# Optimization experiments

Hardware: AMD Instinct MI355X
Metric: run time of the kernel (lower is better)

The kernel has to match this reference:

```python
import jax, jax.numpy as jnp
import numpy as np

N_NODES = 32768
N_GRAPHS = 8
NODES_PER_GRAPH = N_NODES // N_GRAPHS
DEG = 8
N_EDGES = N_NODES * DEG
TW = 25
H = 128
N_LAYERS = 6
L_PDE = 16.0
TMAX = 4.0
DT = 0.04
EPS = 1e-5


def swish(x):
    return x * jax.nn.sigmoid(x)


def _lin(k, fin, fout):
    kw, kb = jax.random.split(k)
    s = 1.0 / np.sqrt(fin)
    return (jax.random.uniform(kw, (fin, fout), minval=-s, maxval=s),
            jax.random.uniform(kb, (fout,), minval=-s, maxval=s))


def _lin_stack(k, n, fin, fout):
    Ws, bs = [], []
    for kk in jax.random.split(k, n):
        W, b = _lin(kk, fin, fout)
        Ws.append(W); bs.append(b)
    return jnp.stack(Ws), jnp.stack(bs)


def setup_inputs() -> dict:
    key = jax.random.key(0)
    ks = jax.random.split(key, 16)
    emb_in = 2 * TW + 2        # 52 = u(50) + pos_x(1) + pos_t(1)
    msg_in = 2 * H + 2 * TW + 2  # 308 = x_i,x_j,u_i-u_j,dpos_x,vars_i
    upd_in = 2 * H + 1          # 257 = x, message, vars
    inp = {}
    inp['u'] = jax.random.normal(ks[0], (N_NODES, 2 * TW), dtype=jnp.float32)
    pos_t = jax.random.uniform(ks[1], (N_NODES, 1)) * TMAX
    pos_x = jax.random.uniform(ks[2], (N_NODES, 1)) * L_PDE
    inp['pos'] = jnp.concatenate([pos_t, pos_x], axis=-1)
    src = jax.random.randint(ks[3], (N_EDGES,), 0, N_NODES)
    dst = jnp.repeat(jnp.arange(N_NODES), DEG)  # every node gets DEG in-edges
    inp['edge_index'] = jnp.stack([src, dst]).astype(jnp.int32)
    inp['batch_idx'] = (jnp.arange(N_NODES) // NODES_PER_GRAPH).astype(jnp.int32)
    inp['emb_W1'], inp['emb_b1'] = _lin(ks[4], emb_in, H)
    inp['emb_W2'], inp['emb_b2'] = _lin(ks[5], H, H)
    inp['msg1_W'], inp['msg1_b'] = _lin_stack(ks[6], N_LAYERS, msg_in, H)
    inp['msg2_W'], inp['msg2_b'] = _lin_stack(ks[7], N_LAYERS, H, H)
    inp['upd1_W'], inp['upd1_b'] = _lin_stack(ks[8], N_LAYERS, upd_in, H)
    inp['upd2_W'], inp['upd2_b'] = _lin_stack(ks[9], N_LAYERS, H, H)
    inp['dbl_W'], inp['dbl_b'] = _lin(ks[10], H, 2 * H)
    kc = jax.random.split(ks[11], 4)
    s1 = 1.0 / np.sqrt(2 * 16)
    inp['conv1_W'] = jax.random.uniform(kc[0], (8, 2, 16), minval=-s1, maxval=s1)
    inp['conv1_b'] = jax.random.uniform(kc[1], (8,), minval=-s1, maxval=s1)
    s2 = 1.0 / np.sqrt(8 * 14)
    inp['conv2_W'] = jax.random.uniform(kc[2], (2, 8, 14), minval=-s2, maxval=s2)
    inp['conv2_b'] = jax.random.uniform(kc[3], (2,), minval=-s2, maxval=s2)
    return inp


def reference(u, pos, edge_index, batch_idx, emb_W1, emb_b1, emb_W2, emb_b2,
              msg1_W, msg1_b, msg2_W, msg2_b, upd1_W, upd1_b, upd2_W, upd2_b,
              dbl_W, dbl_b, conv1_W, conv1_b, conv2_W, conv2_b):
    src, dst = edge_index[0], edge_index[1]  # PyG: x_j = x[src], x_i = x[dst]
    pos_x = pos[:, 1:2] / L_PDE
    pos_t = pos[:, 0:1] / TMAX
    variables = pos_t  # eq_variables == {} -> only pos_t
    node_in = jnp.concatenate([u, pos_x, variables], axis=-1)  # [N,52]
    h = swish(swish(node_in @ emb_W1 + emb_b1) @ emb_W2 + emb_b2)
    ones_e = jnp.ones((src.shape[0], 1), u.dtype)
    counts = jnp.maximum(jax.ops.segment_sum(ones_e, dst, N_NODES), 1.0)
    ones_n = jnp.ones((N_NODES, 1), u.dtype)
    gcounts = jax.ops.segment_sum(ones_n, batch_idx, N_GRAPHS)
    u_d = u[dst] - u[src]
    px_d = pos_x[dst] - pos_x[src]
    var_i = variables[dst]

    def layer(hc, p):
        Wm1, bm1, Wm2, bm2, Wu1, bu1, Wu2, bu2 = p
        edge_in = jnp.concatenate([hc[dst], hc[src], u_d, px_d, var_i], -1)  # [E,308]
        m = swish(edge_in @ Wm1 + bm1)
        m = swish(m @ Wm2 + bm2)
        agg = jax.ops.segment_sum(m, dst, N_NODES) / counts  # mean aggregation
        up = swish(jnp.concatenate([hc, agg, variables], -1) @ Wu1 + bu1)
        up = swish(up @ Wu2 + bu2)
        hn = hc + up  # residual (in_features == out_features)
        gm = jax.ops.segment_sum(hn, batch_idx, N_GRAPHS) / gcounts
        hd = hn - gm[batch_idx]
        gv = jax.ops.segment_sum(hd * hd, batch_idx, N_GRAPHS) / gcounts
        return hd * jax.lax.rsqrt(gv + EPS)[batch_idx], None

    h, _ = jax.lax.scan(layer, h, (msg1_W, msg1_b, msg2_W, msg2_b,
                                   upd1_W, upd1_b, upd2_W, upd2_b))
    x2 = swish(h @ dbl_W + dbl_b).reshape(N_NODES, 2, H)  # double_mlp + Unflatten
    dn = ('NCH', 'OIH', 'NCH')
    y = jax.lax.conv_general_dilated(x2, conv1_W, (3,), 'VALID', dimension_numbers=dn)
    y = swish(y + conv1_b[None, :, None])  # [N,8,38]
    diff = jax.lax.conv_general_dilated(y, conv2_W, (1,), 'VALID', dimension_numbers=dn)
    diff = diff + conv2_b[None, :, None]  # [N,2,25]
    dt_cum = DT * jnp.arange(1, TW + 1, dtype=u.dtype)  # cumsum(dt*ones)
    out = u.reshape(N_NODES, 2, TW) + dt_cum[None, None, :] * diff
    return out.reshape(N_NODES, 2 * TW)
```

## Files before the change

kernel.cpp:

```cpp
#include <hip/hip_runtime.h>
#include <hip/hip_bf16.h>

#define N_NODES 32768
#define N_GRAPHS 8
#define NPG 4096
#define DEG 8
#define N_EDGES (N_NODES*DEG)
#define TW 25
#define NL 6
#define L_PDE 16.0f
#define TMAXC 4.0f
#define DTC 0.04f
#define EPSC 1e-5f

typedef __bf16 bf16x8 __attribute__((ext_vector_type(8)));
typedef float f32x4 __attribute__((ext_vector_type(4)));
typedef unsigned short u16;
typedef unsigned int u32;

__device__ __forceinline__ float bf2f(u16 h){
  union { float f; u32 u; } v; v.u = ((u32)h) << 16; return v.f;
}
__device__ __forceinline__ u16 f2bf(float f){
  union { float f; u32 u; } v; v.f = f;
  u32 r = v.u + 0x7FFFu + ((v.u >> 16) & 1u);
  return (u16)(r >> 16);
}
__device__ __forceinline__ float swishf(float x){
  return x / (1.0f + __expf(-x));
}

__global__ void prep_std(const float* __restrict__ src, u16* __restrict__ dst,
                         int Ksrc, int KPAD, int NOUT)
{
  int l = blockIdx.y;
  int per = KPAD * NOUT;
  int i = blockIdx.x * 256 + threadIdx.x;
  if (i >= per) return;
  int KSTEPS = KPAD / 32;
  int e = i & 7;
  int lane = (i >> 3) & 63;
  int ks = (i >> 9) % KSTEPS;
  int nf = i / (KSTEPS * 512);
  int c = nf * 16 + (lane & 15);
  int k = ks * 32 + (lane >> 4) * 8 + e;
  float v = (k < Ksrc) ? src[(size_t)l * Ksrc * NOUT + (size_t)k * NOUT + c] : 0.f;
  dst[(size_t)l * per + i] = f2bf(v);
}

__global__ void prep_AB(const float* __restrict__ W, const float* __restrict__ bsrc,
                        u16* __restrict__ dst, float* __restrict__ bdst)
{
  int l = blockIdx.y;
  const int KSTEPS = 6;
  int i = blockIdx.x * 256 + threadIdx.x;
  int e = i & 7, lane = (i >> 3) & 63, ks = (i >> 9) % KSTEPS, nf = i / (KSTEPS * 512);
  int c = nf * 16 + (lane & 15);
  int k = ks * 32 + (lane >> 4) * 8 + e;
  const float* Wl = W + (size_t)l * 308 * 128;
  float v = 0.f;
  if (c < 128) {
    int rowi = -1;
    if (k < 128) rowi = k;
    else if (k < 178) rowi = 256 + (k - 128);
    else if (k == 178) rowi = 306;
    else if (k == 179) rowi = 307;
    if (rowi >= 0) v = Wl[rowi * 128 + c];
  } else {
    int cc = c - 128; float sgn = 1.f; int rowi = -1;
    if (k < 128) rowi = 128 + k;
    else if (k < 178) { rowi = 256 + (k - 128); sgn = -1.f; }
    else if (k == 178) { rowi = 306; sgn = -1.f; }
    if (rowi >= 0) v = sgn * Wl[rowi * 128 + cc];
  }
  dst[(size_t)l * 192 * 256 + i] = f2bf(v);
  if (i < 256) bdst[l * 256 + i] = (i < 128) ? bsrc[l * 128 + i] : 0.f;
}

__global__ __launch_bounds__(256) void build_static(
    const float* __restrict__ u, const float* __restrict__ pos,
    u16* __restrict__ X0)
{
  int idx = blockIdx.x * 256 + threadIdx.x;
  int n = idx >> 6, j = idx & 63;
  float v;
  if (j < 50) v = u[n * 50 + j];
  else if (j == 50) v = pos[n * 2 + 1] * (1.f / L_PDE);
  else if (j == 51) v = pos[n * 2 + 0] * (1.f / TMAXC);
  else v = 0.f;
  X0[n * 64 + j] = f2bf(v);
}

template<int KPAD, int NOUT, int ACT, int SMODE, int RESID, int HASOUT>
__global__ __launch_bounds__(256) void gemm2(
    const u16* __restrict__ X, int ldx,
    const u16* __restrict__ Xaux,
    float* hB,
    const float* __restrict__ S1p, const float* __restrict__ S2p,
    const float* __restrict__ pos,
    const u16* __restrict__ Wf, const float* __restrict__ bias,
    u16* __restrict__ out, int ldo,
    float* __restrict__ outF,
    float* __restrict__ S1n, float* __restrict__ S2n)
{
  constexpr int KSTEPS = KPAD / 32;
  constexpr int NF2 = NOUT / 32;
  constexpr int CHUNKS = KPAD / 8;
  constexpr int LDO_S = NOUT + 8;
  constexpr int SMEM_US = 64 * (HASOUT ? (KPAD > LDO_S ? KPAD : LDO_S) : KPAD);
  __shared__ u16 sm[SMEM_US];
  int tid = threadIdx.x, lane = tid & 63, wid = tid >> 6;
  int n0 = blockIdx.x * 64;
  int g = n0 >> 12;

  for (int c = tid; c < 64 * CHUNKS; c += 256) {
    int r = c / CHUNKS, kc = c % CHUNKS;
    int n = n0 + r;
    union { uint4 v; u16 s[8]; } o;
    if (SMODE == 0) {
      o.v = *(const uint4*)(X + (size_t)n * ldx + kc * 8);
    } else {
      if (kc < 16) {
        const float* hp = hB + (size_t)n * 128 + kc * 8;
        float4 a0 = *(const float4*)hp, a1 = *(const float4*)(hp + 4);
        float xv[8] = {a0.x,a0.y,a0.z,a0.w,a1.x,a1.y,a1.z,a1.w};
        if (S1p) {
          #pragma unroll
          for (int j = 0; j < 8; ++j) {
            int cc = kc * 8 + j;
            float m = S1p[g * 128 + cc] * (1.f / NPG);
            float var = S2p[g * 128 + cc] * (1.f / NPG) - m * m;
            xv[j] = (xv[j] - m) * rsqrtf(var + EPSC);
          }
        }
        #pragma unroll
        for (int j = 0; j < 8; ++j) o.s[j] = f2bf(xv[j]);
      } else {
        o.v = *(const uint4*)(Xaux + (size_t)n * 64 + (kc - 16) * 8);
      }
    }
    int byte = r * (KPAD * 2) + kc * 16; byte ^= ((r & 7) << 4);
    *(uint4*)((char*)sm + byte) = o.v;
  }
  __syncthreads();

  int rowHalf = wid & 1, colHalf = wid >> 1;
  f32x4 acc[2][NF2];
  f32x4 zero = {0.f, 0.f, 0.f, 0.f};
  #pragma unroll
  for (int m = 0; m < 2; ++m)
    #pragma unroll
    for (int i = 0; i < NF2; ++i) acc[m][i] = zero;
  int rowA = rowHalf * 32 + (lane & 15);
  int kb = lane >> 4;
  #pragma unroll
  for (int ks = 0; ks < KSTEPS; ++ks) {
    int ab0 = rowA * (KPAD * 2) + ks * 64 + kb * 16; ab0 ^= ((rowA & 7) << 4);
    int rA1 = rowA + 16;
    int ab1 = rA1 * (KPAD * 2) + ks * 64 + kb * 16; ab1 ^= ((rA1 & 7) << 4);
    bf16x8 a0 = *(const bf16x8*)((const char*)sm + ab0);
    bf16x8 a1 = *(const bf16x8*)((const char*)sm + ab1);
    #pragma unroll
    for (int nf2 = 0; nf2 < NF2; ++nf2) {
      bf16x8 b = *(const bf16x8*)(Wf + (((colHalf * NF2 + nf2) * KSTEPS + ks) * 64 + lane) * 8);
      acc[0][nf2] = __builtin_amdgcn_mfma_f32_16x16x32_bf16(a0, b, acc[0][nf2], 0, 0, 0);
      acc[1][nf2] = __builtin_amdgcn_mfma_f32_16x16x32_bf16(a1, b, acc[1][nf2], 0, 0, 0);
    }
  }

  if (HASOUT) __syncthreads();
  #pragma unroll
  for (int nf2 = 0; nf2 < NF2; ++nf2) {
    int col = colHalf * (NOUT / 2) + nf2 * 16 + (lane & 15);
    float bv = bias[col];
    #pragma unroll
    for (int m = 0; m < 2; ++m)
      #pragma unroll
      for (int j = 0; j < 4; ++j) {
        int r = rowHalf * 32 + m * 16 + (lane >> 4) * 4 + j;
        float v = acc[m][nf2][j] + bv;
        if (ACT == 1) v = swishf(v);
        if (HASOUT) sm[r * LDO_S + col] = f2bf(v);
        if (outF) outF[(size_t)(n0 + r) * NOUT + col] = v;
      }
  }
  if (HASOUT) {
    __syncthreads();
    for (int c = tid; c < 64 * NOUT / 8; c += 256) {
      int r = c / (NOUT / 8), kc = c % (NOUT / 8);
      uint4 v = *(const uint4*)(sm + r * LDO_S + kc * 8);
      *(uint4*)(out + (size_t)(n0 + r) * ldo + kc * 8) = v;
    }
  }
}

__global__ __launch_bounds__(256) void enc_fused(
    const u16* __restrict__ X0,
    const u16* __restrict__ W1f, const float* __restrict__ b1,
    const u16* __restrict__ W2f, const float* __restrict__ b2,
    float* __restrict__ hB)
{
  __shared__ u16 s1[64 * 64];
  __shared__ u16 s2[64 * 128];
  int tid = threadIdx.x, lane = tid & 63, wid = tid >> 6;
  int n0 = blockIdx.x * 64;

  for (int c = tid; c < 64 * 8; c += 256) {
    int r = c >> 3, kc = c & 7;
    uint4 v = *(const uint4*)(X0 + (size_t)(n0 + r) * 64 + kc * 8);
    int byte = r * 128 + kc * 16; byte ^= ((r & 7) << 4);
    *(uint4*)((char*)s1 + byte) = v;
  }
  __syncthreads();

  int rowHalf = wid & 1, colHalf = wid >> 1;
  int rowA = rowHalf * 32 + (lane & 15), kb = lane >> 4;
  f32x4 acc[2][4];
  f32x4 zero = {0.f, 0.f, 0.f, 0.f};
  #pragma unroll
  for (int m = 0; m < 2; ++m)
    #pragma unroll
    for (int i = 0; i < 4; ++i) acc[m][i] = zero;
  #pragma unroll
  for (int ks = 0; ks < 2; ++ks) {
    int ab0 = rowA * 128 + ks * 64 + kb * 16; ab0 ^= ((rowA & 7) << 4);
    int rA1 = rowA + 16;
    int ab1 = rA1 * 128 + ks * 64 + kb * 16; ab1 ^= ((rA1 & 7) << 4);
    bf16x8 a0 = *(const bf16x8*)((const char*)s1 + ab0);
    bf16x8 a1 = *(const bf16x8*)((const char*)s1 + ab1);
    #pragma unroll
    for (int nf2 = 0; nf2 < 4; ++nf2) {
      bf16x8 b = *(const bf16x8*)(W1f + (((colHalf * 4 + nf2) * 2 + ks) * 64 + lane) * 8);
      acc[0][nf2] = __builtin_amdgcn_mfma_f32_16x16x32_bf16(a0, b, acc[0][nf2], 0, 0, 0);
      acc[1][nf2] = __builtin_amdgcn_mfma_f32_16x16x32_bf16(a1, b, acc[1][nf2], 0, 0, 0);
    }
  }
  #pragma unroll
  for (int nf2 = 0; nf2 < 4; ++nf2) {
    int col = colHalf * 64 + nf2 * 16 + (lane & 15);
    float bv = b1[col];
    #pragma unroll
    for (int m = 0; m < 2; ++m)
      #pragma unroll
      for (int j = 0; j < 4; ++j) {
        int r = rowHalf * 32 + m * 16 + (lane >> 4) * 4 + j;
        int byte = r * 256 + col * 2; byte ^= ((r & 7) << 4);
        *(u16*)((char*)s2 + byte) = f2bf(swishf(acc[m][nf2][j] + bv));
      }
  }
  __syncthreads();
  #pragma unroll
  for (int m = 0; m < 2; ++m)
    #pragma unroll
    for (int i = 0; i < 4; ++i) acc[m][i] = zero;
  #pragma unroll
  for (int ks = 0; ks < 4; ++ks) {
    int ab0 = rowA * 256 + ks * 64 + kb * 16; ab0 ^= ((rowA & 7) << 4);
    int rA1 = rowA + 16;
    int ab1 = rA1 * 256 + ks * 64 + kb * 16; ab1 ^= ((rA1 & 7) << 4);
    bf16x8 a0 = *(const bf16x8*)((const char*)s2 + ab0);
    bf16x8 a1 = *(const bf16x8*)((const char*)s2 + ab1);
    #pragma unroll
    for (int nf2 = 0; nf2 < 4; ++nf2) {
      bf16x8 b = *(const bf16x8*)(W2f + (((colHalf * 4 + nf2) * 4 + ks) * 64 + lane) * 8);
      acc[0][nf2] = __builtin_amdgcn_mfma_f32_16x16x32_bf16(a0, b, acc[0][nf2], 0, 0, 0);
      acc[1][nf2] = __builtin_amdgcn_mfma_f32_16x16x32_bf16(a1, b, acc[1][nf2], 0, 0, 0);
    }
  }
  #pragma unroll
  for (int nf2 = 0; nf2 < 4; ++nf2) {
    int col = colHalf * 64 + nf2 * 16 + (lane & 15);
    float bv = b2[col];
    #pragma unroll
    for (int m = 0; m < 2; ++m)
      #pragma unroll
      for (int j = 0; j < 4; ++j) {
        int r = rowHalf * 32 + m * 16 + (lane >> 4) * 4 + j;
        hB[(size_t)(n0 + r) * 128 + col] = swishf(acc[m][nf2][j] + bv);
      }
  }
}

__global__ __launch_bounds__(256) void upd_fused(
    const u16* __restrict__ Agg,
    float* hB,
    const float* __restrict__ S1p, const float* __restrict__ S2p,
    const float* __restrict__ pos,
    const u16* __restrict__ W1f, const float* __restrict__ b1,
    const u16* __restrict__ W2f, const float* __restrict__ b2,
    float* __restrict__ S1n, float* __restrict__ S2n)
{
  __shared__ u16 s1[64 * 320];
  __shared__ u16 s2[64 * 128];
  int tid = threadIdx.x, lane = tid & 63, wid = tid >> 6;
  int n0 = blockIdx.x * 64;
  int g = n0 >> 12;

  for (int c = tid; c < 64 * 40; c += 256) {
    int r = c / 40, kc = c % 40;
    int n = n0 + r;
    union { uint4 v; u16 s[8]; } o;
    if (kc < 16) {
      const float* hp = hB + (size_t)n * 128 + kc * 8;
      float4 a0 = *(const float4*)hp, a1 = *(const float4*)(hp + 4);
      float xv[8] = {a0.x,a0.y,a0.z,a0.w,a1.x,a1.y,a1.z,a1.w};
      if (S1p) {
        #pragma unroll
        for (int j = 0; j < 8; ++j) {
          int cc = kc * 8 + j;
          float m = S1p[g * 128 + cc] * (1.f / NPG);
          float var = S2p[g * 128 + cc] * (1.f / NPG) - m * m;
          xv[j] = (xv[j] - m) * rsqrtf(var + EPSC);
        }
      }
      #pragma unroll
      for (int j = 0; j < 8; ++j) o.s[j] = f2bf(xv[j]);
    } else if (kc < 32) {
      o.v = *(const uint4*)(Agg + (size_t)n * 128 + (kc - 16) * 8);
    } else {
      #pragma unroll
      for (int j = 0; j < 8; ++j) o.s[j] = 0;
      if (kc == 32) o.s[0] = f2bf(pos[n * 2] * (1.f / TMAXC));
    }
    int byte = r * 640 + kc * 16; byte ^= ((r & 7) << 4);
    *(uint4*)((char*)s1 + byte) = o.v;
  }
  __syncthreads();

  int rowHalf = wid & 1, colHalf = wid >> 1;
  int rowA = rowHalf * 32 + (lane & 15), kb = lane >> 4;
  f32x4 acc[2][4];
  f32x4 zero = {0.f, 0.f, 0.f, 0.f};
  #pragma unroll
  for (int m = 0; m < 2; ++m)
    #pragma unroll
    for (int i = 0; i < 4; ++i) acc[m][i] = zero;
  #pragma unroll
  for (int ks = 0; ks < 10; ++ks) {
    int ab0 = rowA * 640 + ks * 64 + kb * 16; ab0 ^= ((rowA & 7) << 4);
    int rA1 = rowA + 16;
    int ab1 = rA1 * 640 + ks * 64 + kb * 16; ab1 ^= ((rA1 & 7) << 4);
    bf16x8 a0 = *(const bf16x8*)((const char*)s1 + ab0);
    bf16x8 a1 = *(const bf16x8*)((const char*)s1 + ab1);
    #pragma unroll
    for (int nf2 = 0; nf2 < 4; ++nf2) {
      bf16x8 b = *(const bf16x8*)(W1f + (((colHalf * 4 + nf2) * 10 + ks) * 64 + lane) * 8);
      acc[0][nf2] = __builtin_amdgcn_mfma_f32_16x16x32_bf16(a0, b, acc[0][nf2], 0, 0, 0);
      acc[1][nf2] = __builtin_amdgcn_mfma_f32_16x16x32_bf16(a1, b, acc[1][nf2], 0, 0, 0);
    }
  }
  #pragma unroll
  for (int nf2 = 0; nf2 < 4; ++nf2) {
    int col = colHalf * 64 + nf2 * 16 + (lane & 15);
    float bv = b1[col];
    #pragma unroll
    for (int m = 0; m < 2; ++m)
      #pragma unroll
      for (int j = 0; j < 4; ++j) {
        int r = rowHalf * 32 + m * 16 + (lane >> 4) * 4 + j;
        int byte = r * 256 + col * 2; byte ^= ((r & 7) << 4);
        *(u16*)((char*)s2 + byte) = f2bf(swishf(acc[m][nf2][j] + bv));
      }
  }
  __syncthreads();
  #pragma unroll
  for (int m = 0; m < 2; ++m)
    #pragma unroll
    for (int i = 0; i < 4; ++i) acc[m][i] = zero;
  #pragma unroll
  for (int ks = 0; ks < 4; ++ks) {
    int ab0 = rowA * 256 + ks * 64 + kb * 16; ab0 ^= ((rowA & 7) << 4);
    int rA1 = rowA + 16;
    int ab1 = rA1 * 256 + ks * 64 + kb * 16; ab1 ^= ((rA1 & 7) << 4);
    bf16x8 a0 = *(const bf16x8*)((const char*)s2 + ab0);
    bf16x8 a1 = *(const bf16x8*)((const char*)s2 + ab1);
    #pragma unroll
    for (int nf2 = 0; nf2 < 4; ++nf2) {
      bf16x8 b = *(const bf16x8*)(W2f + (((colHalf * 4 + nf2) * 4 + ks) * 64 + lane) * 8);
      acc[0][nf2] = __builtin_amdgcn_mfma_f32_16x16x32_bf16(a0, b, acc[0][nf2], 0, 0, 0);
      acc[1][nf2] = __builtin_amdgcn_mfma_f32_16x16x32_bf16(a1, b, acc[1][nf2], 0, 0, 0);
    }
  }
  float s1l[4], s2l[4];
  #pragma unroll
  for (int i = 0; i < 4; ++i) { s1l[i] = 0.f; s2l[i] = 0.f; }
  #pragma unroll
  for (int nf2 = 0; nf2 < 4; ++nf2) {
    int col = colHalf * 64 + nf2 * 16 + (lane & 15);
    float bv = b2[col];
    float mm = 0.f, rsig = 1.f;
    if (S1p) {
      mm = S1p[g * 128 + col] * (1.f / NPG);
      float var = S2p[g * 128 + col] * (1.f / NPG) - mm * mm;
      rsig = rsqrtf(var + EPSC);
    }
    #pragma unroll
    for (int m = 0; m < 2; ++m)
      #pragma unroll
      for (int j = 0; j < 4; ++j) {
        int r = rowHalf * 32 + m * 16 + (lane >> 4) * 4 + j;
        int n = n0 + r;
        float v = swishf(acc[m][nf2][j] + bv);
        float hc = hB[(size_t)n * 128 + col];
        hc = (hc - mm) * rsig;
        float hn = hc + v;
        hB[(size_t)n * 128 + col] = hn;
        s1l[nf2] += hn; s2l[nf2] += hn * hn;
      }
  }
  #pragma unroll
  for (int nf2 = 0; nf2 < 4; ++nf2) {
    float s1v = s1l[nf2], s2v = s2l[nf2];
    s1v += __shfl_xor(s1v, 16); s1v += __shfl_xor(s1v, 32);
    s2v += __shfl_xor(s2v, 16); s2v += __shfl_xor(s2v, 32);
    if ((lane >> 4) == 0) {
      int col = colHalf * 64 + nf2 * 16 + (lane & 15);
      atomicAdd(&S1n[g * 128 + col], s1v);
      atomicAdd(&S2n[g * 128 + col], s2v);
    }
  }
}

__global__ __launch_bounds__(256) void msg_kernel(
    const u16* __restrict__ AB, const int* __restrict__ srcIdx,
    const u16* __restrict__ Wf, const float* __restrict__ bm2,
    u16* __restrict__ Agg)
{
  __shared__ u16 Ms[64 * 128];
  __shared__ float aggS[8][132];
  int tid = threadIdx.x, lane = tid & 63, wid = tid >> 6;
  int e0 = blockIdx.x * 64;
  for (int c = tid; c < 1024; c += 256) {
    int i = c >> 4, kc = c & 15;
    int e = e0 + i;
    int nd = e >> 3;
    int ns = srcIdx[e];
    union { uint4 v; u16 s[8]; } va, vb, vo;
    va.v = *(const uint4*)(AB + (size_t)nd * 256 + kc * 8);
    vb.v = *(const uint4*)(AB + (size_t)ns * 256 + 128 + kc * 8);
    #pragma unroll
    for (int j = 0; j < 8; ++j) vo.s[j] = f2bf(swishf(bf2f(va.s[j]) + bf2f(vb.s[j])));
    int byte = i * 256 + kc * 16; byte ^= ((i & 7) << 4);
    *(uint4*)((char*)Ms + byte) = vo.v;
  }
  __syncthreads();
  int rowHalf = wid & 1, colHalf = wid >> 1;
  f32x4 acc[2][4];
  f32x4 zero = {0.f, 0.f, 0.f, 0.f};
  #pragma unroll
  for (int m = 0; m < 2; ++m)
    #pragma unroll
    for (int i = 0; i < 4; ++i) acc[m][i] = zero;
  int rowA = rowHalf * 32 + (lane & 15), kb = lane >> 4;
  #pragma unroll
  for (int ks = 0; ks < 4; ++ks) {
    int ab0 = rowA * 256 + ks * 64 + kb * 16; ab0 ^= ((rowA & 7) << 4);
    int rA1 = rowA + 16;
    int ab1 = rA1 * 256 + ks * 64 + kb * 16; ab1 ^= ((rA1 & 7) << 4);
    bf16x8 a0 = *(const bf16x8*)((const char*)Ms + ab0);
    bf16x8 a1 = *(const bf16x8*)((const char*)Ms + ab1);
    #pragma unroll
    for (int nf2 = 0; nf2 < 4; ++nf2) {
      bf16x8 b = *(const bf16x8*)(Wf + (((colHalf * 4 + nf2) * 4 + ks) * 64 + lane) * 8);
      acc[0][nf2] = __builtin_amdgcn_mfma_f32_16x16x32_bf16(a0, b, acc[0][nf2], 0, 0, 0);
      acc[1][nf2] = __builtin_amdgcn_mfma_f32_16x16x32_bf16(a1, b, acc[1][nf2], 0, 0, 0);
    }
  }
  #pragma unroll
  for (int m = 0; m < 2; ++m)
    #pragma unroll
    for (int nf2 = 0; nf2 < 4; ++nf2) {
      int col = colHalf * 64 + nf2 * 16 + (lane & 15);
      float bv = bm2[col];
      float s = 0.f;
      #pragma unroll
      for (int j = 0; j < 4; ++j) s += swishf(acc[m][nf2][j] + bv);
      s += __shfl_xor(s, 16);
      if ((lane & 31) < 16)
        aggS[rowHalf * 4 + m * 2 + (lane >> 5)][col] = s * 0.125f;
    }
  __syncthreads();
  {
    int node = tid >> 5;
    int c0 = (tid & 31) * 4;
    int n = (e0 >> 3) + node;
    ushort4 o;
    o.x = f2bf(aggS[node][c0 + 0]);
    o.y = f2bf(aggS[node][c0 + 1]);
    o.z = f2bf(aggS[node][c0 + 2]);
    o.w = f2bf(aggS[node][c0 + 3]);
    *(ushort4*)(Agg + (size_t)n * 128 + c0) = o;
  }
}

__global__ __launch_bounds__(256) void dec_conv(
    const float* __restrict__ x2f, const float* __restrict__ u,
    const float* __restrict__ w1, const float* __restrict__ b1,
    const float* __restrict__ w2, const float* __restrict__ b2,
    float* __restrict__ outp)
{
  __shared__ float xs[32 * 260];
  int tid = threadIdx.x;
  int o = tid & 7;
  int nn = tid >> 3;
  int n0 = blockIdx.x * 32;
  int n = n0 + nn;

  for (int i = tid; i < 32 * 64; i += 256) {
    int r = i >> 6, c = i & 63;
    float4 v = *(const float4*)(x2f + (size_t)(n0 + r) * 256 + c * 4);
    *(float4*)(xs + r * 260 + c * 4) = v;
  }
  __syncthreads();

  float b1v = b1[o];
  float y[38];
  #pragma unroll
  for (int t = 0; t < 38; ++t) y[t] = b1v;

  #pragma unroll
  for (int cc = 0; cc < 2; ++cc) {
    float w1r[16];
    {
      const float4* wp = (const float4*)(w1 + o * 32 + cc * 16);
      #pragma unroll
      for (int i = 0; i < 4; ++i) {
        float4 v = wp[i];
        w1r[i*4+0]=v.x; w1r[i*4+1]=v.y; w1r[i*4+2]=v.z; w1r[i*4+3]=v.w;
      }
    }
    const float4* xp = (const float4*)(xs + nn * 260 + cc * 128);
    #pragma unroll
    for (int ch = 0; ch < 32; ++ch) {
      float4 xv = xp[ch];
      float xe[4] = {xv.x, xv.y, xv.z, xv.w};
      #pragma unroll
      for (int e = 0; e < 4; ++e) {
        const int j = ch * 4 + e;
        #pragma unroll
        for (int k = 0; k < 16; ++k) {
          const int tm = j - k;
          if (tm >= 0 && (tm % 3) == 0 && (tm / 3) < 38)
            y[tm / 3] += xe[e] * w1r[k];
        }
      }
    }
  }
  #pragma unroll
  for (int t = 0; t < 38; ++t) y[t] = swishf(y[t]);

  float w2r[28];
  #pragma unroll
  for (int c = 0; c < 2; ++c)
    #pragma unroll
    for (int k = 0; k < 14; ++k)
      w2r[c*14 + k] = w2[(c*8 + o)*14 + k];
  float b2r0 = b2[0], b2r1 = b2[1];

  #pragma unroll
  for (int i = 0; i < 50; ++i) {
    const int c = i / 25, t = i % 25;
    float p = 0.f;
    #pragma unroll
    for (int k = 0; k < 14; ++k) p += y[t + k] * w2r[c*14 + k];
    p += __shfl_xor(p, 1);
    p += __shfl_xor(p, 2);
    p += __shfl_xor(p, 4);
    if (o == (i & 7)) {
      int gi = n * 50 + i;
      float diff = p + (c ? b2r1 : b2r0);
      outp[gi] = u[gi] + (DTC * (t + 1)) * diff;
    }
  }
}

extern "C" void kernel_launch(void* const* d_in, const int* in_sizes, int n_in,
                              void* d_out, int out_size, void* d_ws, size_t ws_size,
                              hipStream_t stream) {
  const float* u     = (const float*)d_in[0];
  const float* pos   = (const float*)d_in[1];
  const int*   eidx  = (const int*)d_in[2];
  const float* embW1 = (const float*)d_in[4];
  const float* embb1 = (const float*)d_in[5];
  const float* embW2 = (const float*)d_in[6];
  const float* embb2 = (const float*)d_in[7];
  const float* m1W   = (const float*)d_in[8];
  const float* m1b   = (const float*)d_in[9];
  const float* m2W   = (const float*)d_in[10];
  const float* m2b   = (const float*)d_in[11];
  const float* u1W   = (const float*)d_in[12];
  const float* u1b   = (const float*)d_in[13];
  const float* u2W   = (const float*)d_in[14];
  const float* u2b   = (const float*)d_in[15];
  const float* dblW  = (const float*)d_in[16];
  const float* dblb  = (const float*)d_in[17];
  const float* c1W   = (const float*)d_in[18];
  const float* c1b   = (const float*)d_in[19];
  const float* c2W   = (const float*)d_in[20];
  const float* c2b   = (const float*)d_in[21];
  float* outp = (float*)d_out;
  const int* srcI = eidx;

  char* ws = (char*)d_ws;
  size_t off = 0;
  auto alloc = [&](size_t bytes) -> char* {
    char* p = ws + off; off += (bytes + 255) & ~(size_t)255; return p;
  };
  u16* X0    = (u16*)alloc((size_t)N_NODES * 64 * 2);
  u16* ABbuf = (u16*)alloc((size_t)N_NODES * 256 * 2);
  u16* Agg   = (u16*)alloc((size_t)N_NODES * 128 * 2);
  float* hB  = (float*)alloc((size_t)N_NODES * 128 * 4);
  float* x2f = (float*)alloc((size_t)N_NODES * 256 * 4);
  float* stats = (float*)alloc((size_t)NL * 2 * 1024 * 4);
  u16* WembF1 = (u16*)alloc(64 * 128 * 2);
  u16* WembF2 = (u16*)alloc(128 * 128 * 2);
  u16* WABf   = (u16*)alloc((size_t)6 * 192 * 256 * 2);
  float* bABf = (float*)alloc(6 * 256 * 4);
  u16* Wm2f   = (u16*)alloc((size_t)6 * 128 * 128 * 2);
  u16* Wu1f   = (u16*)alloc((size_t)6 * 320 * 128 * 2);
  u16* Wu2f   = (u16*)alloc((size_t)6 * 128 * 128 * 2);
  u16* Wdblf  = (u16*)alloc((size_t)128 * 256 * 2);

  hipMemsetAsync(stats, 0, (size_t)NL * 2 * 1024 * 4, stream);

  prep_std<<<dim3(32, 1), 256, 0, stream>>>(embW1, WembF1, 52, 64, 128);
  prep_std<<<dim3(64, 1), 256, 0, stream>>>(embW2, WembF2, 128, 128, 128);
  prep_std<<<dim3(64, 6), 256, 0, stream>>>(m2W, Wm2f, 128, 128, 128);
  prep_std<<<dim3(160, 6), 256, 0, stream>>>(u1W, Wu1f, 257, 320, 128);
  prep_std<<<dim3(64, 6), 256, 0, stream>>>(u2W, Wu2f, 128, 128, 128);
  prep_std<<<dim3(128, 1), 256, 0, stream>>>(dblW, Wdblf, 128, 128, 256);
  prep_AB<<<dim3(192, 6), 256, 0, stream>>>(m1W, m1b, WABf, bABf);
  build_static<<<N_NODES * 64 / 256, 256, 0, stream>>>(u, pos, X0);

  enc_fused<<<512, 256, 0, stream>>>(X0, WembF1, embb1, WembF2, embb2, hB);

  for (int l = 0; l < NL; ++l) {
    const float* S1p = l ? stats + (size_t)(l - 1) * 2048 : nullptr;
    const float* S2p = l ? stats + (size_t)(l - 1) * 2048 + 1024 : nullptr;
    float* S1n = stats + (size_t)l * 2048;
    float* S2n = S1n + 1024;
    gemm2<192, 256, 0, 1, 0, 1><<<512, 256, 0, stream>>>(
        nullptr, 0, X0, hB, S1p, S2p, nullptr,
        WABf + (size_t)l * 192 * 256, bABf + l * 256, ABbuf, 256,
        nullptr, nullptr, nullptr);
    msg_kernel<<<N_EDGES / 64, 256, 0, stream>>>(
        ABbuf, srcI, Wm2f + (size_t)l * 128 * 128, m2b + l * 128, Agg);
    upd_fused<<<512, 256, 0, stream>>>(
        Agg, hB, S1p, S2p, pos,
        Wu1f + (size_t)l * 320 * 128, u1b + l * 128,
        Wu2f + (size_t)l * 128 * 128, u2b + l * 128,
        S1n, S2n);
  }

  gemm2<128, 256, 1, 1, 0, 0><<<512, 256, 0, stream>>>(
      nullptr, 0, nullptr, hB, stats + (size_t)5 * 2048, stats + (size_t)5 * 2048 + 1024,
      nullptr, Wdblf, dblb, nullptr, 0, x2f, nullptr, nullptr);
  dec_conv<<<N_NODES / 32, 256, 0, stream>>>(x2f, u, c1W, c1b, c2W, c2b, outp);
}
```

Baseline: 730.7 us.

## Restructure decoder conv kernel to stage intermediates in shared memory

```diff
diff --git a/kernel.cpp b/kernel.cpp
--- a/kernel.cpp
+++ b/kernel.cpp
@@ -499,77 +499,56 @@
     const float* __restrict__ w2, const float* __restrict__ b2,
     float* __restrict__ outp)
 {
-  __shared__ float xs[32 * 260];
+  __shared__ float xs[16][260];
+  __shared__ float ys[16][8][41];
+  __shared__ float w1s[256], w2s[224];
   int tid = threadIdx.x;
-  int o = tid & 7;
-  int nn = tid >> 3;
-  int n0 = blockIdx.x * 32;
-  int n = n0 + nn;
-
-  for (int i = tid; i < 32 * 64; i += 256) {
+  int n0 = blockIdx.x * 16;
+
+  w1s[tid] = w1[tid];
+  if (tid < 224) w2s[tid] = w2[tid];
+  for (int i = tid; i < 16 * 64; i += 256) {
     int r = i >> 6, c = i & 63;
-    float4 v = *(const float4*)(x2f + (size_t)(n0 + r) * 256 + c * 4);
-    *(float4*)(xs + r * 260 + c * 4) = v;
-  }
-  __syncthreads();
-
-  float b1v = b1[o];
-  float y[38];
-  #pragma unroll
-  for (int t = 0; t < 38; ++t) y[t] = b1v;
-
-  #pragma unroll
-  for (int cc = 0; cc < 2; ++cc) {
-    float w1r[16];
-    {
-      const float4* wp = (const float4*)(w1 + o * 32 + cc * 16);
-      #pragma unroll
-      for (int i = 0; i < 4; ++i) {
-        float4 v = wp[i];
-        w1r[i*4+0]=v.x; w1r[i*4+1]=v.y; w1r[i*4+2]=v.z; w1r[i*4+3]=v.w;
-      }
-    }
-    const float4* xp = (const float4*)(xs + nn * 260 + cc * 128);
-    #pragma unroll
-    for (int ch = 0; ch < 32; ++ch) {
-      float4 xv = xp[ch];
-      float xe[4] = {xv.x, xv.y, xv.z, xv.w};
-      #pragma unroll
-      for (int e = 0; e < 4; ++e) {
-        const int j = ch * 4 + e;
+    *(float4*)(&xs[r][c * 4]) = *(const float4*)(x2f + (size_t)(n0 + r) * 256 + c * 4);
+  }
+  __syncthreads();
+
+  {
+    int n = tid >> 4;
+    int o = (tid >> 1) & 7;
+    int th = tid & 1;
+    float b1v = b1[o];
+    float wA[16], wB[16];
+    #pragma unroll
+    for (int k = 0; k < 16; ++k) { wA[k] = w1s[o * 32 + k]; wB[k] = w1s[o * 32 + 16 + k]; }
+    int tEnd = th * 19 + 19;
+    for (int t = th * 19; t < tEnd; ++t) {
+      float acc = b1v;
+      const float* xa = &xs[n][3 * t];
+      const float* xb = &xs[n][128 + 3 * t];
+      #pragma unroll
+      for (int k = 0; k < 16; ++k) acc += xa[k] * wA[k] + xb[k] * wB[k];
+      ys[n][o][t] = swishf(acc);
+    }
+  }
+  __syncthreads();
+
+  {
+    int n = tid >> 4;
+    int c = (tid >> 3) & 1;
+    int ts = tid & 7;
+    float b2v = b2[c];
+    for (int t = ts; t < 25; t += 8) {
+      float acc = b2v;
+      #pragma unroll
+      for (int ic = 0; ic < 8; ++ic) {
+        const float* yp = &ys[n][ic][t];
+        const float* wp = &w2s[c * 112 + ic * 14];
         #pragma unroll
-        for (int k = 0; k < 16; ++k) {
-          const int tm = j - k;
-          if (tm >= 0 && (tm % 3) == 0 && (tm / 3) < 38)
-            y[tm / 3] += xe[e] * w1r[k];
-        }
-      }
-    }
-  }
-  #pragma unroll
-  for (int t = 0; t < 38; ++t) y[t] = swishf(y[t]);
-
-  float w2r[28];
-  #pragma unroll
-  for (int c = 0; c < 2; ++c)
-    #pragma unroll
-    for (int k = 0; k < 14; ++k)
-      w2r[c*14 + k] = w2[(c*8 + o)*14 + k];
-  float b2r0 = b2[0], b2r1 = b2[1];
-
-  #pragma unroll
-  for (int i = 0; i < 50; ++i) {
-    const int c = i / 25, t = i % 25;
-    float p = 0.f;
-    #pragma unroll
-    for (int k = 0; k < 14; ++k) p += y[t + k] * w2r[c*14 + k];
-    p += __shfl_xor(p, 1);
-    p += __shfl_xor(p, 2);
-    p += __shfl_xor(p, 4);
-    if (o == (i & 7)) {
-      int gi = n * 50 + i;
-      float diff = p + (c ? b2r1 : b2r0);
-      outp[gi] = u[gi] + (DTC * (t + 1)) * diff;
+        for (int k = 0; k < 14; ++k) acc += yp[k] * wp[k];
+      }
+      int gi = (n0 + n) * 50 + c * 25 + t;
+      outp[gi] = u[gi] + (DTC * (t + 1)) * acc;
     }
   }
 }
@@ -655,5 +634,5 @@
   gemm2<128, 256, 1, 1, 0, 0><<<512, 256, 0, stream>>>(
       nullptr, 0, nullptr, hB, stats + (size_t)5 * 2048, stats + (size_t)5 * 2048 + 1024,
       nullptr, Wdblf, dblb, nullptr, 0, x2f, nullptr, nullptr);
-  dec_conv<<<N_NODES / 32, 256, 0, stream>>>(x2f, u, c1W, c1b, c2W, c2b, outp);
-}
+  dec_conv<<<N_NODES / 16, 256, 0, stream>>>(x2f, u, c1W, c1b, c2W, c2b, outp);
+}
```

Measured after the change: 711.0 us. -2.7%, faster.
